# Performance work log

Measured on AMD Instinct MI355X. Metric: run time of the kernel, lower is better.

Reference implementation:

```python
import jax, jax.numpy as jnp
import numpy as np

B, C, H, W = 16, 64, 256, 256
WS = 4  # window_size


def setup_inputs() -> dict:
    key = jax.random.key(0)
    k = jax.random.split(key, 5)
    c2, c4 = C // 2, C // 4
    return {
        "x": jax.random.normal(k[0], (B, C, H, W), dtype=jnp.float32),
        "w1": jax.random.normal(k[1], (c2, C), dtype=jnp.float32) * 0.05,
        "b1": jax.random.normal(k[2], (c2,), dtype=jnp.float32) * 0.05,
        "w2": jax.random.normal(k[3], (C, c4), dtype=jnp.float32) * 0.05,
        "b2": jax.random.normal(k[4], (C,), dtype=jnp.float32) * 0.05,
    }


def reference(x, w1, b1, w2, b2):
    b, c, h, w = x.shape
    ws = WS
    c2, c4 = c // 2, c // 4
    bnum = ws * ws                      # 16 windows positions
    l = (h // ws) * (w // ws)           # tokens per position

    # inp: 1x1 conv c->c/2 + ReLU
    x_ = jax.nn.relu(jnp.einsum('oc,bchw->bohw', w1, x) + b1[None, :, None, None])

    # rearrange 'b c (h dh) (w dw) -> b c (dh dw) (h w)', dh=dw=4
    qx = x_.reshape(b, c2, h // ws, ws, w // ws, ws)
    qx = qx.transpose(0, 1, 3, 5, 2, 4).reshape(b, c2, bnum, l)

    vx = qx[:, c4:]                     # [b, c/4, 16, l]

    # windowed mean + (buggy, faithful) 3rd moment: divisor is bnum (dim-2 size), not l
    mean = qx.mean(-1, keepdims=True)                    # [b, c/2, 16, 1]
    m3 = ((qx - mean) ** 3).sum(-1, keepdims=True) / bnum
    qkv = mean + m3

    q, v = qkv[:, :c4], qkv[:, c4:]     # each [b, c/4, 16, 1]

    atn = jax.nn.softmax(q @ jnp.swapaxes(q, -1, -2), axis=-1)  # [b, c/4, 16, 16]
    y = atn @ v                                                 # [b, c/4, 16, 1]

    Fv = vx * jax.nn.sigmoid(y)         # broadcast gate over l

    # inverse rearrange 'b c (dh dw) (h w) -> b c (h dh) (w dw)'
    Fv = Fv.reshape(b, c4, ws, ws, h // ws, w // ws)
    Fv = Fv.transpose(0, 1, 4, 2, 5, 3).reshape(b, c4, h, w)

    out = jnp.einsum('oc,bchw->bohw', w2, Fv) + b2[None, :, None, None]
    return out + x
```

## Files before the change

kernel.cpp:

```cpp
#include <hip/hip_runtime.h>
#include <hip/hip_bf16.h>

#define NB 16
#define NC 64
#define C2 32
#define C4 16
#define HH 256
#define WW 256
#define HW (HH*WW)

typedef unsigned short u16;
typedef u16 u16x8 __attribute__((ext_vector_type(8)));


__global__ __launch_bounds__(256) void prep_kernel(const float* __restrict__ w1,
                                                   float* __restrict__ ws) {
    int t = threadIdx.x;
    for (int i = t; i < 2048; i += 256) {
        int o = i >> 6, c = i & 63;
        ws[c * 32 + o] = w1[i];
    }
}

__global__ __launch_bounds__(256) void conv_kernel(const float* __restrict__ x,
                                                   const float* __restrict__ w1t,
                                                   const float* __restrict__ b1,
                                                   u16* __restrict__ y) {
    int bh = blockIdx.x;
    int b  = bh >> 8;
    int h  = bh & 255;
    int w  = threadIdx.x;
    const float* xb = x + (size_t)b * NC * HW + h * WW + w;

    float xr[64];
    #pragma unroll
    for (int c = 0; c < 64; c++) xr[c] = xb[(size_t)c * HW];

    float acc[32];
    #pragma unroll
    for (int o = 0; o < 32; o++) acc[o] = b1[o];
    #pragma unroll
    for (int c = 0; c < 64; c++) {
        float xc = xr[c];
        #pragma unroll
        for (int o = 0; o < 32; o++) acc[o] += w1t[c * 32 + o] * xc;
    }

    int s = (h & 3) * 4 + (w & 3);
    int l = (h >> 2) * 64 + (w >> 2);
    u16* yb = y + (size_t)b * (32 * 16 * 4096) + s * 4096 + l;
    #pragma unroll
    for (int o = 0; o < 32; o++) {
        float v = fmaxf(acc[o], 0.f);
        __hip_bfloat16 hv = __float2bfloat16(v);
        yb[(size_t)o * 65536] = *reinterpret_cast<u16*>(&hv);
    }
}

__global__ __launch_bounds__(256) void qkv_kernel(const u16* __restrict__ y,
                                                  float* __restrict__ qkv) {
    int g    = blockIdx.x * 4 + (threadIdx.x >> 6);
    int lane = threadIdx.x & 63;
    const u16x8* p = (const u16x8*)(y + (size_t)g * 4096);

    float S1 = 0.f, S2 = 0.f, S3 = 0.f;
    #pragma unroll
    for (int k = 0; k < 8; k++) {
        u16x8 v8 = p[k * 64 + lane];
        #pragma unroll
        for (int j = 0; j < 8; j++) {
            unsigned int bits = (unsigned int)v8[j] << 16;
            float v = __builtin_bit_cast(float, bits);
            S1 += v;
            float pw = v * v;
            S2 += pw;
            S3 += pw * v;
        }
    }
    #pragma unroll
    for (int m = 1; m <= 32; m <<= 1) {
        S1 += __shfl_xor(S1, m);
        S2 += __shfl_xor(S2, m);
        S3 += __shfl_xor(S3, m);
    }
    if (lane == 0) {
        float mu = S1 * (1.f / 4096.f);
        float m3 = (S3 - 3.f * mu * S2 + 2.f * 4096.f * mu * mu * mu) * (1.f / 16.f);
        qkv[g] = mu + m3;
    }
}

__global__ __launch_bounds__(512) void attn_kernel(const float* __restrict__ qkvg,
                                                   float* __restrict__ gates) {
    int b = blockIdx.x;
    int t = threadIdx.x;
    __shared__ float qkv[512];
    qkv[t] = qkvg[b * 512 + t];
    __syncthreads();
    if (t < 256) {
        int o = t >> 4, s = t & 15;
        float qs = qkv[o * 16 + s];
        float mx = -1e30f;
        #pragma unroll
        for (int k = 0; k < 16; k++) mx = fmaxf(mx, qs * qkv[o * 16 + k]);
        float sum = 0.f, y = 0.f;
        #pragma unroll
        for (int k = 0; k < 16; k++) {
            float e = __expf(qs * qkv[o * 16 + k] - mx);
            sum += e;
            y   += e * qkv[(16 + o) * 16 + k];
        }
        y /= sum;
        float g = 1.f / (1.f + __expf(-y));
        gates[b * 256 + o * 16 + s] = g;
    }
}

__global__ __launch_bounds__(256) void out_kernel(const float* __restrict__ x,
                                                  const float* __restrict__ w1t,
                                                  const float* __restrict__ b1,
                                                  const float* __restrict__ w2,
                                                  const float* __restrict__ b2,
                                                  const float* __restrict__ gates,
                                                  float* __restrict__ out) {
    int bh = blockIdx.x;
    int b  = bh >> 8;
    int h  = bh & 255;
    int w  = threadIdx.x;
    int s  = (h & 3) * 4 + (w & 3);
    const float* xb = x   + (size_t)b * NC * HW + h * WW + w;
    float*       ob = out + (size_t)b * NC * HW + h * WW + w;

    __shared__ float gsh[256];
    gsh[w] = gates[b * 256 + w];
    __syncthreads();

    float xr[64];
    #pragma unroll
    for (int c = 0; c < 64; c++) xr[c] = xb[(size_t)c * HW];

    float fv[16];
    #pragma unroll
    for (int j = 0; j < 16; j++) fv[j] = b1[16 + j];
    #pragma unroll
    for (int c = 0; c < 64; c++) {
        float xc = xr[c];
        #pragma unroll
        for (int j = 0; j < 16; j++) fv[j] += w1t[c * 32 + 16 + j] * xc;
    }
    #pragma unroll
    for (int j = 0; j < 16; j++) {
        float v = fv[j] > 0.f ? fv[j] : 0.f;
        fv[j] = v * gsh[j * 16 + s];
    }
    #pragma unroll
    for (int o = 0; o < 64; o++) {
        float r = b2[o] + xr[o];
        #pragma unroll
        for (int j = 0; j < 16; j++) r += w2[o * 16 + j] * fv[j];
        ob[(size_t)o * HW] = r;
    }
}

extern "C" void kernel_launch(void* const* d_in, const int* in_sizes, int n_in,
                              void* d_out, int out_size, void* d_ws, size_t ws_size,
                              hipStream_t stream) {
    const float* x  = (const float*)d_in[0];
    const float* w1 = (const float*)d_in[1];
    const float* b1 = (const float*)d_in[2];
    const float* w2 = (const float*)d_in[3];
    const float* b2 = (const float*)d_in[4];
    float* ws    = (float*)d_ws;
    float* w1t   = ws;
    float* qkv   = ws + 2048;
    float* gates = ws + 26624;
    u16*   y     = (u16*)(ws + 32768);
    float* out   = (float*)d_out;

    prep_kernel<<<1,    256, 0, stream>>>(w1, ws);
    conv_kernel<<<4096, 256, 0, stream>>>(x, w1t, b1, y);
    qkv_kernel <<<2048, 256, 0, stream>>>(y, qkv);
    attn_kernel<<<16,   512, 0, stream>>>(qkv, gates);
    out_kernel <<<4096, 256, 0, stream>>>(x, w1t, b1, w2, b2, gates, out);
}
```

Measured before the change: 248.9 us.

## Store conv output in natural layout and reduce window positions in qkv kernel

The conv kernel now writes the bf16 intermediate in plain (b,c,h,w) order instead of the scattered window-position layout. Each thread's store is therefore coalesced along w rather than strided by 4. The qkv kernel now does one (b,c) plane per block and keeps 4x4 per-position accumulators split by h&3 and w&3. It combines them with shuffles and a small shared-memory step. This targets the uncoalesced store pattern in conv, at the cost of a more involved reduction and fewer, larger qkv blocks.

```diff
diff --git a/kernel.cpp b/kernel.cpp
--- a/kernel.cpp
+++ b/kernel.cpp
@@ -46,47 +46,74 @@
         for (int o = 0; o < 32; o++) acc[o] += w1t[c * 32 + o] * xc;
     }
 
-    int s = (h & 3) * 4 + (w & 3);
-    int l = (h >> 2) * 64 + (w >> 2);
-    u16* yb = y + (size_t)b * (32 * 16 * 4096) + s * 4096 + l;
+    u16* yb = y + (size_t)b * (32 * HW) + h * WW + w;
     #pragma unroll
     for (int o = 0; o < 32; o++) {
         float v = fmaxf(acc[o], 0.f);
         __hip_bfloat16 hv = __float2bfloat16(v);
-        yb[(size_t)o * 65536] = *reinterpret_cast<u16*>(&hv);
+        yb[(size_t)o * HW] = *reinterpret_cast<u16*>(&hv);
     }
 }
 
 __global__ __launch_bounds__(256) void qkv_kernel(const u16* __restrict__ y,
                                                   float* __restrict__ qkv) {
-    int g    = blockIdx.x * 4 + (threadIdx.x >> 6);
-    int lane = threadIdx.x & 63;
-    const u16x8* p = (const u16x8*)(y + (size_t)g * 4096);
-
-    float S1 = 0.f, S2 = 0.f, S3 = 0.f;
-    #pragma unroll
-    for (int k = 0; k < 8; k++) {
-        u16x8 v8 = p[k * 64 + lane];
+    int g    = blockIdx.x;
+    int t    = threadIdx.x;
+    int wave = t >> 6;
+    int lane = t & 63;
+    int half = lane >> 5;
+    int hres = (wave * 2 + half) & 3;
+    const u16x8* p = (const u16x8*)(y + (size_t)g * HW);
+
+    float S1[4], S2[4], S3[4];
+    #pragma unroll
+    for (int j = 0; j < 4; j++) { S1[j] = 0.f; S2[j] = 0.f; S3[j] = 0.f; }
+
+    #pragma unroll 4
+    for (int k = 0; k < 32; ++k) {
+        int h = k * 8 + wave * 2 + half;
+        u16x8 v8 = p[h * 32 + (lane & 31)];
         #pragma unroll
         for (int j = 0; j < 8; j++) {
             unsigned int bits = (unsigned int)v8[j] << 16;
             float v = __builtin_bit_cast(float, bits);
-            S1 += v;
+            int wr = j & 3;
+            S1[wr] += v;
             float pw = v * v;
-            S2 += pw;
-            S3 += pw * v;
-        }
-    }
-    #pragma unroll
-    for (int m = 1; m <= 32; m <<= 1) {
-        S1 += __shfl_xor(S1, m);
-        S2 += __shfl_xor(S2, m);
-        S3 += __shfl_xor(S3, m);
-    }
-    if (lane == 0) {
-        float mu = S1 * (1.f / 4096.f);
-        float m3 = (S3 - 3.f * mu * S2 + 2.f * 4096.f * mu * mu * mu) * (1.f / 16.f);
-        qkv[g] = mu + m3;
+            S2[wr] += pw;
+            S3[wr] += pw * v;
+        }
+    }
+
+    #pragma unroll
+    for (int wr = 0; wr < 4; wr++) {
+        #pragma unroll
+        for (int m = 1; m <= 16; m <<= 1) {
+            S1[wr] += __shfl_xor(S1[wr], m);
+            S2[wr] += __shfl_xor(S2[wr], m);
+            S3[wr] += __shfl_xor(S3[wr], m);
+        }
+    }
+
+    __shared__ float red[2][4][4][3];
+    if ((lane & 31) == 0) {
+        int src = wave >> 1;
+        #pragma unroll
+        for (int wr = 0; wr < 4; wr++) {
+            red[src][hres][wr][0] = S1[wr];
+            red[src][hres][wr][1] = S2[wr];
+            red[src][hres][wr][2] = S3[wr];
+        }
+    }
+    __syncthreads();
+    if (t < 16) {
+        int hr = t >> 2, wr = t & 3;
+        float s1 = red[0][hr][wr][0] + red[1][hr][wr][0];
+        float s2 = red[0][hr][wr][1] + red[1][hr][wr][1];
+        float s3 = red[0][hr][wr][2] + red[1][hr][wr][2];
+        float mu = s1 * (1.f / 4096.f);
+        float m3 = (s3 - 3.f * mu * s2 + 2.f * 4096.f * mu * mu * mu) * (1.f / 16.f);
+        qkv[g * 16 + t] = mu + m3;
     }
 }
 
@@ -179,7 +206,7 @@
 
     prep_kernel<<<1,    256, 0, stream>>>(w1, ws);
     conv_kernel<<<4096, 256, 0, stream>>>(x, w1t, b1, y);
-    qkv_kernel <<<2048, 256, 0, stream>>>(y, qkv);
+    qkv_kernel <<<512,  256, 0, stream>>>(y, qkv);
     attn_kernel<<<16,   512, 0, stream>>>(qkv, gates);
     out_kernel <<<4096, 256, 0, stream>>>(x, w1t, b1, w2, b2, gates, out);
 }
```

After: 248.1 us. About the same (-0.3%).
